# Optimization experiments

Measured on AMD Instinct MI355X. Metric: run time of the kernel, lower is better.

## Reference

```python
import jax, jax.numpy as jnp
import numpy as np

B, N, T, CIN, HID, EMB, K = 32, 256, 13, 2, 64, 10, 2


def setup_inputs() -> dict:
    key = jax.random.key(0)
    ks = jax.random.split(key, 24)
    r = lambda i, shape, s=1.0: jax.random.normal(ks[i], shape, jnp.float32) * s
    return {
        "times": jnp.arange(T, dtype=jnp.float32),
        # natural cubic spline coefficients: (B, N, T-1, CIN)
        "coeff_a": r(0, (B, N, T - 1, CIN)),
        "coeff_b": r(1, (B, N, T - 1, CIN), 0.1),
        "coeff_two_c": r(2, (B, N, T - 1, CIN), 0.1),
        "coeff_three_d": r(3, (B, N, T - 1, CIN), 0.1),
        # initial_h / initial_z linear layers (input -> hidden)
        "W_h": r(4, (CIN, HID), 0.5), "b_h": r(5, (HID,), 0.1),
        "W_z": r(6, (CIN, HID), 0.5), "b_z": r(7, (HID,), 0.1),
        # func_f (FinalTanh_f): linear_in, one hidden linear, linear_out -> hidden*input
        "Wf_in": r(8, (HID, HID), 0.1), "bf_in": r(9, (HID,), 0.05),
        "Wf_hid": r(10, (HID, HID), 0.1), "bf_hid": r(11, (HID,), 0.05),
        "Wf_out": r(12, (HID, HID * CIN), 0.1), "bf_out": r(13, (HID * CIN,), 0.05),
        # func_g (VectorField_g, g_type='agc')
        "Wg_in": r(14, (HID, HID), 0.1), "bg_in": r(15, (HID,), 0.05),
        "Eg": r(16, (N, EMB)),
        "W_pool": r(17, (EMB, K, HID, HID), 0.1),
        "b_pool": r(18, (EMB, HID), 0.1),
        "Wg_out": r(19, (HID, HID * CIN), 0.1), "bg_out": r(20, (HID * CIN,), 0.05),
    }


def reference(times, coeff_a, coeff_b, coeff_two_c, coeff_three_d,
              W_h, b_h, W_z, b_z,
              Wf_in, bf_in, Wf_hid, bf_hid, Wf_out, bf_out,
              Wg_in, bg_in, Eg, W_pool, b_pool, Wg_out, bg_out):
    maxidx = coeff_b.shape[-2] - 1

    def dX_dt(t):  # NaturalCubicSpline.derivative
        idx = jnp.clip(jnp.searchsorted(times, t, side='right') - 1, 0, maxidx)
        frac = t - times[idx]
        b = coeff_b[..., idx, :]
        c = coeff_two_c[..., idx, :]
        d = coeff_three_d[..., idx, :]
        return b + (c + d * frac) * frac  # (B, N, CIN)

    # adaptive graph conv (agc) static pieces, cheb_k = 2
    A = jax.nn.softmax(jax.nn.relu(Eg @ Eg.T), axis=1)          # (N, N)
    supports = jnp.stack([jnp.eye(N, dtype=A.dtype), A])        # (K, N, N)
    Wn = jnp.einsum('nd,dkio->nkio', Eg, W_pool)                # (N, K, HID, HID)
    bn = Eg @ b_pool                                            # (N, HID)

    def func_f(h):  # FinalTanh_f: MLP -> (B, N, HID, CIN) field
        x = jax.nn.relu(h @ Wf_in + bf_in)
        x = jax.nn.relu(x @ Wf_hid + bf_hid)
        x = (x @ Wf_out + bf_out).reshape(*x.shape[:-1], HID, CIN)
        return jnp.tanh(x)

    def func_g(z):  # VectorField_g with agc
        x = jax.nn.relu(z @ Wg_in + bg_in)                       # (B, N, HID)
        x_g = jnp.einsum('knm,bmc->bnkc', supports, x)           # (B, N, K, HID)
        x = jnp.einsum('bnki,nkio->bno', x_g, Wn) + bn           # (B, N, HID)
        x = (x @ Wg_out + bg_out).reshape(*x.shape[:-1], HID, CIN)
        return jnp.tanh(x)

    def vf(t, h, z):  # VectorField_g_dev of cdeint_gde_dev
        dX = dX_dt(t)                                            # (B, N, CIN)
        f = func_f(h)
        g = func_g(z)
        dh = jnp.einsum('bnhi,bni->bnh', f, dX)
        dz = jnp.einsum('bnhi,bni->bnh', g * f, dX)
        return dh, dz

    # spline.evaluate(times[0]) == coeff_a[..., 0, :] (frac = 0)
    x0 = coeff_a[..., 0, :]
    h0 = x0 @ W_h + b_h
    z0 = x0 @ W_z + b_z

    third = jnp.float32(1.0 / 3.0)

    def step(carry, ts):  # torchdiffeq 'rk4' (3/8 rule), one step per interval
        h, z = carry
        t0, t1 = ts
        dt = t1 - t0
        k1h, k1z = vf(t0, h, z)
        k2h, k2z = vf(t0 + dt * third, h + dt * third * k1h, z + dt * third * k1z)
        k3h, k3z = vf(t0 + dt * 2 * third, h + dt * (k2h - third * k1h), z + dt * (k2z - third * k1z))
        k4h, k4z = vf(t1, h + dt * (k1h - k2h + k3h), z + dt * (k1z - k2z + k3z))
        h = h + dt * 0.125 * (k1h + 3.0 * (k2h + k3h) + k4h)
        z = z + dt * 0.125 * (k1z + 3.0 * (k2z + k3z) + k4z)
        return (h, z), z

    ts = jnp.stack([times[:-1], times[1:]], axis=1)              # (T-1, 2)
    (_, _), z_seq = jax.lax.scan(step, (h0, z0), ts)
    z_t = jnp.concatenate([z0[None], z_seq], axis=0)             # (T, B, N, HID)
    return jnp.transpose(z_t, (1, 2, 0, 3))                      # (B, N, T, HID)
```

## Files before the change

### kernel.cpp

```cpp
#include <hip/hip_runtime.h>

typedef unsigned short ushort_t;
typedef unsigned int uint_t;

#define CW_OFF  0
#define A_OFF   524288
#define BN_OFF  786432
#define WN_OFF  851968
#define XB_OFF  5046272
#define H_OFF   7143424
#define Z_OFF   9240576
#define K1H_OFF 11337728
#define K1Z_OFF 13434880
#define K2H_OFF 15532032
#define K2Z_OFF 17629184
#define UH_OFF  19726336

#define F_X0     0
#define F_WH     16384
#define F_BH     16512
#define F_WZ     16576
#define F_BZ     16704
#define F_WFIN   16768
#define F_BFIN   20864
#define F_WFHID  20928
#define F_BFHID  25024
#define F_WFOUT  25088
#define F_BFOUT  33280
#define F_WGIN   33408
#define F_BGIN   37504
#define F_WGOUT  37568
#define F_BGOUT  45760
#define F_EG     45888
#define F_WPOOL  48448
#define F_BPOOL  130368

__device__ __forceinline__ float bfl(uint_t u){ union{uint_t i; float f;} c; c.i = u<<16; return c.f; }
__device__ __forceinline__ float bfh(uint_t u){ union{uint_t i; float f;} c; c.i = u & 0xffff0000u; return c.f; }
__device__ __forceinline__ float bf1(ushort_t u){ union{uint_t i; float f;} c; c.i = ((uint_t)u)<<16; return c.f; }
__device__ __forceinline__ uint_t f2bf(float x){
  uint_t u = __float_as_uint(x);
  uint_t r = u + 0x7fffu + ((u >> 16) & 1u);
  return r >> 16;
}
__device__ __forceinline__ float fast_tanh(float x){
  float e = __expf(2.0f*x);
  return 1.0f - 2.0f/(e+1.0f);
}
__device__ __forceinline__ bool inputs_are_f32(const void* times){
  return ((const uint_t*)times)[0] != 0x3F800000u;
}

__device__ __forceinline__ void dotf_4(const float* act, const float* W, int o0, float acc[4]) {
  const float4* a4 = (const float4*)act;
  #pragma unroll
  for (int i4 = 0; i4 < 16; ++i4) {
    float4 av4 = a4[i4];
    float av[4] = {av4.x, av4.y, av4.z, av4.w};
    #pragma unroll
    for (int ii = 0; ii < 4; ++ii) {
      float4 w = *(const float4*)(W + (i4*4+ii)*64 + o0);
      acc[0] += av[ii]*w.x; acc[1] += av[ii]*w.y;
      acc[2] += av[ii]*w.z; acc[3] += av[ii]*w.w;
    }
  }
}

__device__ __forceinline__ void dotf_8(const float* act, const float* W, int co0, float acc[8]) {
  const float4* a4 = (const float4*)act;
  #pragma unroll
  for (int i4 = 0; i4 < 16; ++i4) {
    float4 av4 = a4[i4];
    float av[4] = {av4.x, av4.y, av4.z, av4.w};
    #pragma unroll
    for (int ii = 0; ii < 4; ++ii) {
      const float* wp = W + (i4*4+ii)*128 + co0;
      float4 w0 = *(const float4*)(wp);
      float4 w1 = *(const float4*)(wp + 4);
      float a = av[ii];
      acc[0] += a*w0.x; acc[1] += a*w0.y; acc[2] += a*w0.z; acc[3] += a*w0.w;
      acc[4] += a*w1.x; acc[5] += a*w1.y; acc[6] += a*w1.z; acc[7] += a*w1.w;
    }
  }
}

__global__ __launch_bounds__(256) void k_conv(
    const void* times, const void* ca,
    const void* W_h, const void* b_h, const void* W_z, const void* b_z,
    const void* Wf_in, const void* bf_in, const void* Wf_hid, const void* bf_hid,
    const void* Wf_out, const void* bf_out, const void* Wg_in, const void* bg_in,
    const void* Wg_out, const void* bg_out, const void* Eg, const void* W_pool,
    const void* b_pool, char* __restrict__ wsb)
{
  const bool f32in = inputs_are_f32(times);
  float* F = (float*)(wsb + CW_OFF);
  if (blockIdx.x == 0) {
    for (int i = threadIdx.x; i < 16384; i += 256) {
      int si = (i >> 1)*24 + (i & 1);
      F[F_X0 + i] = f32in ? ((const float*)ca)[si] : bf1(((const ushort_t*)ca)[si]);
    }
    return;
  }
  const void* src = nullptr; int dst = 0, cnt = 0;
  switch (blockIdx.x) {
    case 1:  src = W_h;    dst = F_WH;    cnt = 128;   break;
    case 2:  src = b_h;    dst = F_BH;    cnt = 64;    break;
    case 3:  src = W_z;    dst = F_WZ;    cnt = 128;   break;
    case 4:  src = b_z;    dst = F_BZ;    cnt = 64;    break;
    case 5:  src = Wf_in;  dst = F_WFIN;  cnt = 4096;  break;
    case 6:  src = bf_in;  dst = F_BFIN;  cnt = 64;    break;
    case 7:  src = Wf_hid; dst = F_WFHID; cnt = 4096;  break;
    case 8:  src = bf_hid; dst = F_BFHID; cnt = 64;    break;
    case 9:  src = Wf_out; dst = F_WFOUT; cnt = 8192;  break;
    case 10: src = bf_out; dst = F_BFOUT; cnt = 128;   break;
    case 11: src = Wg_in;  dst = F_WGIN;  cnt = 4096;  break;
    case 12: src = bg_in;  dst = F_BGIN;  cnt = 64;    break;
    case 13: src = Wg_out; dst = F_WGOUT; cnt = 8192;  break;
    case 14: src = bg_out; dst = F_BGOUT; cnt = 128;   break;
    case 15: src = Eg;     dst = F_EG;    cnt = 2560;  break;
    case 16: src = W_pool; dst = F_WPOOL; cnt = 81920; break;
    default: src = b_pool; dst = F_BPOOL; cnt = 640;   break;
  }
  for (int i = threadIdx.x; i < cnt; i += 256)
    F[dst + i] = f32in ? ((const float*)src)[i] : bf1(((const ushort_t*)src)[i]);
}

__global__ __launch_bounds__(256) void k_A(char* __restrict__ wsb) {
  const float* F = (const float*)(wsb + CW_OFF);
  float* Aw = (float*)(wsb + A_OFF);
  float* bn = (float*)(wsb + BN_OFF);
  const int nrow = blockIdx.x;
  const int m = threadIdx.x;
  float eg_n[10];
  #pragma unroll
  for (int d = 0; d < 10; ++d) eg_n[d] = F[F_EG + nrow*10 + d];
  float dot = 0.f;
  #pragma unroll
  for (int d = 0; d < 10; ++d) dot += eg_n[d] * F[F_EG + m*10 + d];
  float v = fmaxf(dot, 0.f);
  __shared__ float red[256];
  red[m] = v; __syncthreads();
  for (int off = 128; off > 0; off >>= 1) {
    if (m < off) red[m] = fmaxf(red[m], red[m+off]);
    __syncthreads();
  }
  float vmax = red[0]; __syncthreads();
  float e = __expf(v - vmax);
  red[m] = e; __syncthreads();
  for (int off = 128; off > 0; off >>= 1) {
    if (m < off) red[m] += red[m+off];
    __syncthreads();
  }
  float ssum = red[0];
  Aw[nrow*256 + m] = e / ssum;
  if (m < 64) {
    float acc = 0.f;
    #pragma unroll
    for (int d = 0; d < 10; ++d) acc += eg_n[d] * F[F_BPOOL + d*64 + m];
    bn[nrow*64 + m] = acc;
  }
}

__global__ __launch_bounds__(256) void k_Wn(char* __restrict__ wsb) {
  const float* F = (const float*)(wsb + CW_OFF);
  ushort_t* Wn = (ushort_t*)(wsb + WN_OFF);
  int idx = blockIdx.x*256 + threadIdx.x;
  int o = idx & 63;
  int i = (idx >> 6) & 63;
  int k = (idx >> 12) & 1;
  int n = idx >> 13;
  float acc = 0.f;
  #pragma unroll
  for (int d = 0; d < 10; ++d)
    acc += F[F_EG + n*10 + d] * F[F_WPOOL + ((d*2 + k)*64 + i)*64 + o];
  Wn[idx] = (ushort_t)f2bf(acc);
}

__global__ __launch_bounds__(512) void k_init2(char* __restrict__ wsb, float* __restrict__ out) {
  const float* F = (const float*)(wsb + CW_OFF);
  float* H = (float*)(wsb + H_OFF);
  float* Z = (float*)(wsb + Z_OFF);
  ushort_t* X0 = (ushort_t*)(wsb + XB_OFF);

  const int tid = threadIdx.x;
  const int lr  = tid >> 4;
  const int o0  = (tid & 15) * 4;
  const int row = blockIdx.x * 32 + lr;

  __shared__ __align__(16) float sIn[32][68];

  float a0 = F[F_X0 + row*2 + 0];
  float a1 = F[F_X0 + row*2 + 1];
  float h[4], z[4];
  #pragma unroll
  for (int j = 0; j < 4; ++j) {
    h[j] = a0*F[F_WH + o0+j] + a1*F[F_WH + 64+o0+j] + F[F_BH + o0+j];
    z[j] = a0*F[F_WZ + o0+j] + a1*F[F_WZ + 64+o0+j] + F[F_BZ + o0+j];
  }
  *(float4*)(H + row*64 + o0) = make_float4(h[0],h[1],h[2],h[3]);
  *(float4*)(Z + row*64 + o0) = make_float4(z[0],z[1],z[2],z[3]);
  *(float4*)(out + (row*13)*64 + o0) = make_float4(z[0],z[1],z[2],z[3]);

  *(float4*)&sIn[lr][o0] = make_float4(z[0],z[1],z[2],z[3]);
  __syncthreads();
  float xr[4];
  { float4 bv = *(const float4*)(F + F_BGIN + o0);
    xr[0]=bv.x; xr[1]=bv.y; xr[2]=bv.z; xr[3]=bv.w; }
  dotf_4(&sIn[lr][0], F + F_WGIN, o0, xr);
  #pragma unroll
  for (int j=0;j<4;++j) xr[j] = fmaxf(xr[j], 0.f);
  { uint2 pk;
    pk.x = f2bf(xr[0]) | (f2bf(xr[1]) << 16);
    pk.y = f2bf(xr[2]) | (f2bf(xr[3]) << 16);
    *(uint2*)(X0 + row*64 + o0) = pk; }
}

__global__ __launch_bounds__(512) void k_stage(
    const void* __restrict__ times,
    const void* __restrict__ cbv, const void* __restrict__ ccv, const void* __restrict__ cdv,
    char* __restrict__ wsb, float* __restrict__ out, int vfc)
{
  const float* F  = (const float*)(wsb + CW_OFF);
  const float* Aw = (const float*)(wsb + A_OFF);
  const float* bn = (const float*)(wsb + BN_OFF);
  const ushort_t* Wn = (const ushort_t*)(wsb + WN_OFF);
  ushort_t* XB = (ushort_t*)(wsb + XB_OFF);
  float* H   = (float*)(wsb + H_OFF);
  float* Z   = (float*)(wsb + Z_OFF);
  float* K1h = (float*)(wsb + K1H_OFF);
  float* K1z = (float*)(wsb + K1Z_OFF);
  float* K2h = (float*)(wsb + K2H_OFF);
  float* K2z = (float*)(wsb + K2Z_OFF);
  float* UH  = (float*)(wsb + UH_OFF);
  const bool f32in = inputs_are_f32(times);

  const int s  = vfc >> 2;
  const int st = vfc & 3;
  const ushort_t* Xc = XB + (vfc & 1) * 524288;
  ushort_t*       Xn = XB + ((vfc + 1) & 1) * 524288;

  const int tid = threadIdx.x;
  const int lr  = tid >> 4;
  const int t16 = tid & 15;
  const int o0  = t16 * 4;
  const int co0 = o0 * 2;
  const int bb  = blockIdx.x >> 3;
  const int nr  = blockIdx.x & 7;
  const int n   = nr * 32 + lr;
  const int row = bb * 256 + n;

  __shared__ __align__(16) float sIn[32][68];
  __shared__ __align__(16) float sT [32][68];
  __shared__ __align__(16) float sX [32][68];
  __shared__ __align__(16) float xs [128][68];

  { uint2 w = *(const uint2*)(Xc + row*64 + o0);
    *(float4*)&sX[lr][o0] = make_float4(bfl(w.x), bfh(w.x), bfl(w.y), bfh(w.y)); }

  float y[4] = {0.f,0.f,0.f,0.f};
  const float* Arow = Aw + n*256;
  #pragma unroll 1
  for (int half = 0; half < 2; ++half) {
    __syncthreads();
    #pragma unroll
    for (int q = tid; q < 2048; q += 512) {
      int r = q >> 4, c4 = q & 15;
      uint2 w = *(const uint2*)(Xc + (bb*256 + half*128 + r)*64 + c4*4);
      *(float4*)&xs[r][c4*4] = make_float4(bfl(w.x), bfh(w.x), bfl(w.y), bfh(w.y));
    }
    __syncthreads();
    #pragma unroll 4
    for (int m4 = 0; m4 < 32; ++m4) {
      float4 av = *(const float4*)(Arow + half*128 + m4*4);
      float am[4] = {av.x, av.y, av.z, av.w};
      #pragma unroll
      for (int mm = 0; mm < 4; ++mm) {
        float4 xv = *(const float4*)&xs[m4*4+mm][o0];
        y[0] += am[mm]*xv.x; y[1] += am[mm]*xv.y;
        y[2] += am[mm]*xv.z; y[3] += am[mm]*xv.w;
      }
    }
  }

  __syncthreads();
  *(float4*)&sT[lr][o0] = make_float4(y[0],y[1],y[2],y[3]);
  __syncthreads();
  float og[4];
  { float4 bv = *(const float4*)(bn + n*64 + o0); og[0]=bv.x; og[1]=bv.y; og[2]=bv.z; og[3]=bv.w; }
  const ushort_t* W0 = Wn + n*8192;
  #pragma unroll
  for (int i4 = 0; i4 < 16; ++i4) {
    float4 xa = *(const float4*)&sX[lr][i4*4];
    float4 ya = *(const float4*)&sT[lr][i4*4];
    float xav[4]={xa.x,xa.y,xa.z,xa.w};
    float yav[4]={ya.x,ya.y,ya.z,ya.w};
    #pragma unroll
    for (int ii = 0; ii < 4; ++ii) {
      int i = i4*4 + ii;
      uint2 w0 = *(const uint2*)(W0 + i*64 + o0);
      uint2 w1 = *(const uint2*)(W0 + 4096 + i*64 + o0);
      og[0] += xav[ii]*bfl(w0.x) + yav[ii]*bfl(w1.x);
      og[1] += xav[ii]*bfh(w0.x) + yav[ii]*bfh(w1.x);
      og[2] += xav[ii]*bfl(w0.y) + yav[ii]*bfl(w1.y);
      og[3] += xav[ii]*bfh(w0.y) + yav[ii]*bfh(w1.y);
    }
  }
  *(float4*)&sIn[lr][o0] = make_float4(og[0],og[1],og[2],og[3]);
  __syncthreads();
  float go[8];
  { float4 b0 = *(const float4*)(F + F_BGOUT + co0);
    float4 b1 = *(const float4*)(F + F_BGOUT + co0 + 4);
    go[0]=b0.x; go[1]=b0.y; go[2]=b0.z; go[3]=b0.w;
    go[4]=b1.x; go[5]=b1.y; go[6]=b1.z; go[7]=b1.w; }
  dotf_8(&sIn[lr][0], F + F_WGOUT, co0, go);
  float g0[4], g1[4];
  #pragma unroll
  for (int j=0;j<4;++j){ g0[j]=fast_tanh(go[2*j]); g1[j]=fast_tanh(go[2*j+1]); }

  __syncthreads();
  { const float* UHsrc = (st == 0) ? H : UH;
    float4 uv = *(const float4*)(UHsrc + row*64 + o0);
    *(float4*)&sIn[lr][o0] = uv; }
  __syncthreads();
  float a1v[4];
  { float4 bv = *(const float4*)(F + F_BFIN + o0);
    a1v[0]=bv.x; a1v[1]=bv.y; a1v[2]=bv.z; a1v[3]=bv.w; }
  dotf_4(&sIn[lr][0], F + F_WFIN, o0, a1v);
  #pragma unroll
  for (int j=0;j<4;++j) a1v[j] = fmaxf(a1v[j], 0.f);
  *(float4*)&sT[lr][o0] = make_float4(a1v[0],a1v[1],a1v[2],a1v[3]);
  __syncthreads();
  float a2v[4];
  { float4 bv = *(const float4*)(F + F_BFHID + o0);
    a2v[0]=bv.x; a2v[1]=bv.y; a2v[2]=bv.z; a2v[3]=bv.w; }
  dotf_4(&sT[lr][0], F + F_WFHID, o0, a2v);
  #pragma unroll
  for (int j=0;j<4;++j) a2v[j] = fmaxf(a2v[j], 0.f);
  *(float4*)&sIn[lr][o0] = make_float4(a2v[0],a2v[1],a2v[2],a2v[3]);
  __syncthreads();
  float fo[8];
  { float4 b0 = *(const float4*)(F + F_BFOUT + co0);
    float4 b1 = *(const float4*)(F + F_BFOUT + co0 + 4);
    fo[0]=b0.x; fo[1]=b0.y; fo[2]=b0.z; fo[3]=b0.w;
    fo[4]=b1.x; fo[5]=b1.y; fo[6]=b1.z; fo[7]=b1.w; }
  dotf_8(&sIn[lr][0], F + F_WFOUT, co0, fo);
  float f0[4], f1[4];
  #pragma unroll
  for (int j=0;j<4;++j){ f0[j]=fast_tanh(fo[2*j]); f1[j]=fast_tanh(fo[2*j+1]); }

  int sidx; float frac;
  if (st == 0)      { sidx = s; frac = 0.f; }
  else if (st == 1) { sidx = s; frac = 0.33333334f; }
  else if (st == 2) { sidx = s; frac = 0.66666669f; }
  else              { sidx = (s < 11) ? s+1 : 11; frac = (s < 11) ? 0.f : 1.f; }
  float dX0, dX1;
  if (f32in) {
    float2 vb = *(const float2*)((const float*)cbv + (row*12 + sidx)*2);
    float2 vc = *(const float2*)((const float*)ccv + (row*12 + sidx)*2);
    float2 vd = *(const float2*)((const float*)cdv + (row*12 + sidx)*2);
    dX0 = vb.x + (vc.x + vd.x*frac)*frac;
    dX1 = vb.y + (vc.y + vd.y*frac)*frac;
  } else {
    uint_t vb = *(const uint_t*)((const ushort_t*)cbv + (row*12 + sidx)*2);
    uint_t vc = *(const uint_t*)((const ushort_t*)ccv + (row*12 + sidx)*2);
    uint_t vd = *(const uint_t*)((const ushort_t*)cdv + (row*12 + sidx)*2);
    dX0 = bfl(vb) + (bfl(vc) + bfl(vd)*frac)*frac;
    dX1 = bfh(vb) + (bfh(vc) + bfh(vd)*frac)*frac;
  }

  float dh[4], dz[4];
  #pragma unroll
  for (int j=0;j<4;++j){
    dh[j] = f0[j]*dX0 + f1[j]*dX1;
    dz[j] = g0[j]*f0[j]*dX0 + g1[j]*f1[j]*dX1;
  }

  float uh_n[4], uz_n[4];
  float4 hv = *(const float4*)(H + row*64 + o0);
  float4 zv = *(const float4*)(Z + row*64 + o0);
  float h[4] = {hv.x,hv.y,hv.z,hv.w};
  float z[4] = {zv.x,zv.y,zv.z,zv.w};

  if (st == 0) {
    *(float4*)(K1h + row*64 + o0) = make_float4(dh[0],dh[1],dh[2],dh[3]);
    *(float4*)(K1z + row*64 + o0) = make_float4(dz[0],dz[1],dz[2],dz[3]);
    #pragma unroll
    for (int j=0;j<4;++j){ uh_n[j]=h[j]+dh[j]*(1.f/3.f); uz_n[j]=z[j]+dz[j]*(1.f/3.f); }
  } else if (st == 1) {
    float4 k1hv = *(const float4*)(K1h + row*64 + o0);
    float4 k1zv = *(const float4*)(K1z + row*64 + o0);
    float k1hl[4]={k1hv.x,k1hv.y,k1hv.z,k1hv.w};
    float k1zl[4]={k1zv.x,k1zv.y,k1zv.z,k1zv.w};
    float Qh[4],Qz[4],Ph[4],Pz[4];
    #pragma unroll
    for (int j=0;j<4;++j){
      Qh[j]=k1hl[j]+3.f*dh[j]; Qz[j]=k1zl[j]+3.f*dz[j];
      Ph[j]=k1hl[j]-dh[j];     Pz[j]=k1zl[j]-dz[j];
      uh_n[j]=h[j]+dh[j]-k1hl[j]*(1.f/3.f);
      uz_n[j]=z[j]+dz[j]-k1zl[j]*(1.f/3.f);
    }
    *(float4*)(K1h + row*64 + o0) = make_float4(Qh[0],Qh[1],Qh[2],Qh[3]);
    *(float4*)(K1z + row*64 + o0) = make_float4(Qz[0],Qz[1],Qz[2],Qz[3]);
    *(float4*)(K2h + row*64 + o0) = make_float4(Ph[0],Ph[1],Ph[2],Ph[3]);
    *(float4*)(K2z + row*64 + o0) = make_float4(Pz[0],Pz[1],Pz[2],Pz[3]);
  } else if (st == 2) {
    float4 Qhv = *(const float4*)(K1h + row*64 + o0);
    float4 Qzv = *(const float4*)(K1z + row*64 + o0);
    float4 Phv = *(const float4*)(K2h + row*64 + o0);
    float4 Pzv = *(const float4*)(K2z + row*64 + o0);
    float Qh[4]={Qhv.x,Qhv.y,Qhv.z,Qhv.w}, Qz[4]={Qzv.x,Qzv.y,Qzv.z,Qzv.w};
    float Ph[4]={Phv.x,Phv.y,Phv.z,Phv.w}, Pz[4]={Pzv.x,Pzv.y,Pzv.z,Pzv.w};
    float Ah[4],Az[4];
    #pragma unroll
    for (int j=0;j<4;++j){
      Ah[j]=Qh[j]+3.f*dh[j]; Az[j]=Qz[j]+3.f*dz[j];
      uh_n[j]=h[j]+Ph[j]+dh[j];
      uz_n[j]=z[j]+Pz[j]+dz[j];
    }
    *(float4*)(K1h + row*64 + o0) = make_float4(Ah[0],Ah[1],Ah[2],Ah[3]);
    *(float4*)(K1z + row*64 + o0) = make_float4(Az[0],Az[1],Az[2],Az[3]);
  } else {
    float4 Ahv = *(const float4*)(K1h + row*64 + o0);
    float4 Azv = *(const float4*)(K1z + row*64 + o0);
    #pragma unroll
    for (int j=0;j<4;++j){
      float hn = h[j] + 0.125f*(((const float*)&Ahv)[j] + dh[j]);
      float zn = z[j] + 0.125f*(((const float*)&Azv)[j] + dz[j]);
      uh_n[j]=hn; uz_n[j]=zn;
    }
    *(float4*)(H + row*64 + o0) = make_float4(uh_n[0],uh_n[1],uh_n[2],uh_n[3]);
    *(float4*)(Z + row*64 + o0) = make_float4(uz_n[0],uz_n[1],uz_n[2],uz_n[3]);
    *(float4*)(out + (row*13 + s + 1)*64 + o0) = make_float4(uz_n[0],uz_n[1],uz_n[2],uz_n[3]);
  }

  if (vfc < 47) {
    *(float4*)(UH + row*64 + o0) = make_float4(uh_n[0],uh_n[1],uh_n[2],uh_n[3]);
    __syncthreads();
    *(float4*)&sIn[lr][o0] = make_float4(uz_n[0],uz_n[1],uz_n[2],uz_n[3]);
    __syncthreads();
    float xr[4];
    { float4 bv = *(const float4*)(F + F_BGIN + o0);
      xr[0]=bv.x; xr[1]=bv.y; xr[2]=bv.z; xr[3]=bv.w; }
    dotf_4(&sIn[lr][0], F + F_WGIN, o0, xr);
    #pragma unroll
    for (int j=0;j<4;++j) xr[j] = fmaxf(xr[j], 0.f);
    uint2 pk;
    pk.x = f2bf(xr[0]) | (f2bf(xr[1]) << 16);
    pk.y = f2bf(xr[2]) | (f2bf(xr[3]) << 16);
    *(uint2*)(Xn + row*64 + o0) = pk;
  }
}

extern "C" void kernel_launch(void* const* d_in, const int* in_sizes, int n_in,
                              void* d_out, int out_size, void* d_ws, size_t ws_size,
                              hipStream_t stream) {
  const void* times   = d_in[0];
  const void* coeff_a = d_in[1];
  const void* coeff_b = d_in[2];
  const void* coeff_c = d_in[3];
  const void* coeff_d = d_in[4];
  const void* W_h    = d_in[5];
  const void* b_h    = d_in[6];
  const void* W_z    = d_in[7];
  const void* b_z    = d_in[8];
  const void* Wf_in  = d_in[9];
  const void* bf_in  = d_in[10];
  const void* Wf_hid = d_in[11];
  const void* bf_hid = d_in[12];
  const void* Wf_out = d_in[13];
  const void* bf_out = d_in[14];
  const void* Wg_in  = d_in[15];
  const void* bg_in  = d_in[16];
  const void* Eg     = d_in[17];
  const void* W_pool = d_in[18];
  const void* b_pool = d_in[19];
  const void* Wg_out = d_in[20];
  const void* bg_out = d_in[21];

  char* wsb = (char*)d_ws;
  float* out = (float*)d_out;

  hipLaunchKernelGGL(k_conv, dim3(18), dim3(256), 0, stream,
                     times, coeff_a, W_h, b_h, W_z, b_z,
                     Wf_in, bf_in, Wf_hid, bf_hid, Wf_out, bf_out,
                     Wg_in, bg_in, Wg_out, bg_out, Eg, W_pool, b_pool, wsb);
  hipLaunchKernelGGL(k_A,  dim3(256),  dim3(256), 0, stream, wsb);
  hipLaunchKernelGGL(k_Wn, dim3(8192), dim3(256), 0, stream, wsb);
  hipLaunchKernelGGL(k_init2, dim3(256), dim3(512), 0, stream, wsb, out);
  for (int vfc = 0; vfc < 48; ++vfc) {
    hipLaunchKernelGGL(k_stage, dim3(256), dim3(512), 0, stream,
                       times, coeff_b, coeff_c, coeff_d, wsb, out, vfc);
  }
}
```

Before: 5.216 ms.

## Claim stage tiles per XCD via atomic flags and use nontemporal stores

Each k_stage block reads its hardware XCD id and claims a (batch, node-range) tile with atomicCAS on a per-tile flag array. This keeps a given tile on the same XCD across the 48 stage launches so its L2-resident state (H, Z, K buffers) is reused. It also switches write-once or read-once buffers (out, K2h/K2z) to nontemporal loads and stores to reduce cache pollution. The cost is a serialized atomic claim at the start of every block, plus a dependence on the workspace being large enough and on the flag counters staying in step with vfc.

```diff
diff --git a/kernel.cpp b/kernel.cpp
--- a/kernel.cpp
+++ b/kernel.cpp
@@ -2,6 +2,7 @@
 
 typedef unsigned short ushort_t;
 typedef unsigned int uint_t;
+typedef float f4v __attribute__((ext_vector_type(4)));
 
 #define CW_OFF  0
 #define A_OFF   524288
@@ -15,6 +16,8 @@
 #define K2H_OFF 15532032
 #define K2Z_OFF 17629184
 #define UH_OFF  19726336
+#define FLAGS_OFF 21823488
+#define WS_NEED   21824512
 
 #define F_X0     0
 #define F_WH     16384
@@ -51,6 +54,12 @@
   return ((const uint_t*)times)[0] != 0x3F800000u;
 }
 
+__device__ __forceinline__ f4v ntld4(const float* p){ return __builtin_nontemporal_load((const f4v*)p); }
+__device__ __forceinline__ void ntst4(float* p, float a, float b, float c, float d){
+  f4v v; v[0]=a; v[1]=b; v[2]=c; v[3]=d;
+  __builtin_nontemporal_store(v, (f4v*)p);
+}
+
 __device__ __forceinline__ void dotf_4(const float* act, const float* W, int o0, float acc[4]) {
   const float4* a4 = (const float4*)act;
   #pragma unroll
@@ -90,11 +99,15 @@
     const void* Wf_in, const void* bf_in, const void* Wf_hid, const void* bf_hid,
     const void* Wf_out, const void* bf_out, const void* Wg_in, const void* bg_in,
     const void* Wg_out, const void* bg_out, const void* Eg, const void* W_pool,
-    const void* b_pool, char* __restrict__ wsb)
+    const void* b_pool, char* __restrict__ wsb, int claim_en)
 {
   const bool f32in = inputs_are_f32(times);
   float* F = (float*)(wsb + CW_OFF);
   if (blockIdx.x == 0) {
+    if (claim_en) {
+      int* flags = (int*)(wsb + FLAGS_OFF);
+      for (int i = threadIdx.x; i < 256; i += 256) flags[i] = 0;
+    }
     for (int i = threadIdx.x; i < 16384; i += 256) {
       int si = (i >> 1)*24 + (i & 1);
       F[F_X0 + i] = f32in ? ((const float*)ca)[si] : bf1(((const ushort_t*)ca)[si]);
@@ -199,7 +212,7 @@
   }
   *(float4*)(H + row*64 + o0) = make_float4(h[0],h[1],h[2],h[3]);
   *(float4*)(Z + row*64 + o0) = make_float4(z[0],z[1],z[2],z[3]);
-  *(float4*)(out + (row*13)*64 + o0) = make_float4(z[0],z[1],z[2],z[3]);
+  ntst4(out + (row*13)*64 + o0, z[0],z[1],z[2],z[3]);
 
   *(float4*)&sIn[lr][o0] = make_float4(z[0],z[1],z[2],z[3]);
   __syncthreads();
@@ -218,7 +231,7 @@
 __global__ __launch_bounds__(512) void k_stage(
     const void* __restrict__ times,
     const void* __restrict__ cbv, const void* __restrict__ ccv, const void* __restrict__ cdv,
-    char* __restrict__ wsb, float* __restrict__ out, int vfc)
+    char* __restrict__ wsb, float* __restrict__ out, int vfc, int claim_en)
 {
   const float* F  = (const float*)(wsb + CW_OFF);
   const float* Aw = (const float*)(wsb + A_OFF);
@@ -244,8 +257,38 @@
   const int t16 = tid & 15;
   const int o0  = t16 * 4;
   const int co0 = o0 * 2;
-  const int bb  = blockIdx.x >> 3;
-  const int nr  = blockIdx.x & 7;
+
+  int bb, nr;
+  __shared__ int s_slot;
+  if (claim_en) {
+    if (tid == 0) {
+      int* flags = (int*)(wsb + FLAGS_OFF);
+      uint_t x = __builtin_amdgcn_s_getreg((3 << 11) | 20) & 7u;
+      int slot = -1;
+      int start = (int)(blockIdx.x >> 3) & 31;
+      #pragma unroll 1
+      for (int t = 0; t < 32; ++t) {
+        int s2 = (((start + t) & 31) << 3) | (int)x;
+        if (atomicCAS(&flags[s2], vfc, vfc + 1) == vfc) { slot = s2; break; }
+      }
+      #pragma unroll 1
+      while (slot < 0) {
+        #pragma unroll 1
+        for (int t = 0; t < 256; ++t) {
+          int s2 = ((int)blockIdx.x + t) & 255;
+          if (atomicCAS(&flags[s2], vfc, vfc + 1) == vfc) { slot = s2; break; }
+        }
+      }
+      s_slot = slot;
+    }
+    __syncthreads();
+    bb = s_slot >> 3;
+    nr = s_slot & 7;
+  } else {
+    bb = blockIdx.x >> 3;
+    nr = blockIdx.x & 7;
+  }
+
   const int n   = nr * 32 + lr;
   const int row = bb * 256 + n;
 
@@ -401,15 +444,15 @@
     }
     *(float4*)(K1h + row*64 + o0) = make_float4(Qh[0],Qh[1],Qh[2],Qh[3]);
     *(float4*)(K1z + row*64 + o0) = make_float4(Qz[0],Qz[1],Qz[2],Qz[3]);
-    *(float4*)(K2h + row*64 + o0) = make_float4(Ph[0],Ph[1],Ph[2],Ph[3]);
-    *(float4*)(K2z + row*64 + o0) = make_float4(Pz[0],Pz[1],Pz[2],Pz[3]);
+    ntst4(K2h + row*64 + o0, Ph[0],Ph[1],Ph[2],Ph[3]);
+    ntst4(K2z + row*64 + o0, Pz[0],Pz[1],Pz[2],Pz[3]);
   } else if (st == 2) {
     float4 Qhv = *(const float4*)(K1h + row*64 + o0);
     float4 Qzv = *(const float4*)(K1z + row*64 + o0);
-    float4 Phv = *(const float4*)(K2h + row*64 + o0);
-    float4 Pzv = *(const float4*)(K2z + row*64 + o0);
+    f4v Phv = ntld4(K2h + row*64 + o0);
+    f4v Pzv = ntld4(K2z + row*64 + o0);
     float Qh[4]={Qhv.x,Qhv.y,Qhv.z,Qhv.w}, Qz[4]={Qzv.x,Qzv.y,Qzv.z,Qzv.w};
-    float Ph[4]={Phv.x,Phv.y,Phv.z,Phv.w}, Pz[4]={Pzv.x,Pzv.y,Pzv.z,Pzv.w};
+    float Ph[4]={Phv[0],Phv[1],Phv[2],Phv[3]}, Pz[4]={Pzv[0],Pzv[1],Pzv[2],Pzv[3]};
     float Ah[4],Az[4];
     #pragma unroll
     for (int j=0;j<4;++j){
@@ -430,7 +473,7 @@
     }
     *(float4*)(H + row*64 + o0) = make_float4(uh_n[0],uh_n[1],uh_n[2],uh_n[3]);
     *(float4*)(Z + row*64 + o0) = make_float4(uz_n[0],uz_n[1],uz_n[2],uz_n[3]);
-    *(float4*)(out + (row*13 + s + 1)*64 + o0) = make_float4(uz_n[0],uz_n[1],uz_n[2],uz_n[3]);
+    ntst4(out + (row*13 + s + 1)*64 + o0, uz_n[0],uz_n[1],uz_n[2],uz_n[3]);
   }
 
   if (vfc < 47) {
@@ -479,16 +522,17 @@
 
   char* wsb = (char*)d_ws;
   float* out = (float*)d_out;
+  const int claim_en = (ws_size >= (size_t)WS_NEED) ? 1 : 0;
 
   hipLaunchKernelGGL(k_conv, dim3(18), dim3(256), 0, stream,
                      times, coeff_a, W_h, b_h, W_z, b_z,
                      Wf_in, bf_in, Wf_hid, bf_hid, Wf_out, bf_out,
-                     Wg_in, bg_in, Wg_out, bg_out, Eg, W_pool, b_pool, wsb);
+                     Wg_in, bg_in, Wg_out, bg_out, Eg, W_pool, b_pool, wsb, claim_en);
   hipLaunchKernelGGL(k_A,  dim3(256),  dim3(256), 0, stream, wsb);
   hipLaunchKernelGGL(k_Wn, dim3(8192), dim3(256), 0, stream, wsb);
   hipLaunchKernelGGL(k_init2, dim3(256), dim3(512), 0, stream, wsb, out);
   for (int vfc = 0; vfc < 48; ++vfc) {
     hipLaunchKernelGGL(k_stage, dim3(256), dim3(512), 0, stream,
-                       times, coeff_b, coeff_c, coeff_d, wsb, out, vfc);
-  }
-}
+                       times, coeff_b, coeff_c, coeff_d, wsb, out, vfc, claim_en);
+  }
+}
```

After: 5.146 ms. No clear change (-1.3%).

## Remap stage blocks to XCC-local work slots via atomic claims; use nontemporal output stores

Applied to the files above, without the earlier changes.

Each k_stage block reads its XCC id from a hardware register and atomically claims a (batch, node-range) slot whose low bits match that XCC. This keeps each slot on the same XCC across the 48 stage launches so its working set stays in that XCC's L2. Output stores become nontemporal so the write-once output does not evict reused data. The cost is an atomic claim loop at block start, plus a fallback scan when no matching slot is free.

```diff
diff --git a/kernel.cpp b/kernel.cpp
--- a/kernel.cpp
+++ b/kernel.cpp
@@ -2,6 +2,7 @@
 
 typedef unsigned short ushort_t;
 typedef unsigned int uint_t;
+typedef float f4v __attribute__((ext_vector_type(4)));
 
 #define CW_OFF  0
 #define A_OFF   524288
@@ -35,6 +36,8 @@
 #define F_WPOOL  48448
 #define F_BPOOL  130368
 
+__device__ int g_claim[256];
+
 __device__ __forceinline__ float bfl(uint_t u){ union{uint_t i; float f;} c; c.i = u<<16; return c.f; }
 __device__ __forceinline__ float bfh(uint_t u){ union{uint_t i; float f;} c; c.i = u & 0xffff0000u; return c.f; }
 __device__ __forceinline__ float bf1(ushort_t u){ union{uint_t i; float f;} c; c.i = ((uint_t)u)<<16; return c.f; }
@@ -49,6 +52,11 @@
 }
 __device__ __forceinline__ bool inputs_are_f32(const void* times){
   return ((const uint_t*)times)[0] != 0x3F800000u;
+}
+
+__device__ __forceinline__ void ntst4(float* p, float a, float b, float c, float d){
+  f4v v; v[0]=a; v[1]=b; v[2]=c; v[3]=d;
+  __builtin_nontemporal_store(v, (f4v*)p);
 }
 
 __device__ __forceinline__ void dotf_4(const float* act, const float* W, int o0, float acc[4]) {
@@ -95,6 +103,7 @@
   const bool f32in = inputs_are_f32(times);
   float* F = (float*)(wsb + CW_OFF);
   if (blockIdx.x == 0) {
+    if (threadIdx.x < 256) g_claim[threadIdx.x] = 0;
     for (int i = threadIdx.x; i < 16384; i += 256) {
       int si = (i >> 1)*24 + (i & 1);
       F[F_X0 + i] = f32in ? ((const float*)ca)[si] : bf1(((const ushort_t*)ca)[si]);
@@ -199,7 +208,7 @@
   }
   *(float4*)(H + row*64 + o0) = make_float4(h[0],h[1],h[2],h[3]);
   *(float4*)(Z + row*64 + o0) = make_float4(z[0],z[1],z[2],z[3]);
-  *(float4*)(out + (row*13)*64 + o0) = make_float4(z[0],z[1],z[2],z[3]);
+  ntst4(out + (row*13)*64 + o0, z[0],z[1],z[2],z[3]);
 
   *(float4*)&sIn[lr][o0] = make_float4(z[0],z[1],z[2],z[3]);
   __syncthreads();
@@ -244,8 +253,32 @@
   const int t16 = tid & 15;
   const int o0  = t16 * 4;
   const int co0 = o0 * 2;
-  const int bb  = blockIdx.x >> 3;
-  const int nr  = blockIdx.x & 7;
+
+  int bb, nr;
+  __shared__ int s_slot;
+  if (tid == 0) {
+    uint_t x = __builtin_amdgcn_s_getreg((3 << 11) | 20) & 7u;
+    int slot = -1;
+    int start = (int)(blockIdx.x >> 3) & 31;
+    #pragma unroll 1
+    for (int t = 0; t < 32; ++t) {
+      int s2 = (((start + t) & 31) << 3) | (int)x;
+      if (atomicCAS(&g_claim[s2], vfc, vfc + 1) == vfc) { slot = s2; break; }
+    }
+    #pragma unroll 1
+    while (slot < 0) {
+      #pragma unroll 1
+      for (int t = 0; t < 256; ++t) {
+        int s2 = ((int)blockIdx.x + t) & 255;
+        if (atomicCAS(&g_claim[s2], vfc, vfc + 1) == vfc) { slot = s2; break; }
+      }
+    }
+    s_slot = slot;
+  }
+  __syncthreads();
+  bb = s_slot >> 3;
+  nr = s_slot & 7;
+
   const int n   = nr * 32 + lr;
   const int row = bb * 256 + n;
 
@@ -430,7 +463,7 @@
     }
     *(float4*)(H + row*64 + o0) = make_float4(uh_n[0],uh_n[1],uh_n[2],uh_n[3]);
     *(float4*)(Z + row*64 + o0) = make_float4(uz_n[0],uz_n[1],uz_n[2],uz_n[3]);
-    *(float4*)(out + (row*13 + s + 1)*64 + o0) = make_float4(uz_n[0],uz_n[1],uz_n[2],uz_n[3]);
+    ntst4(out + (row*13 + s + 1)*64 + o0, uz_n[0],uz_n[1],uz_n[2],uz_n[3]);
   }
 
   if (vfc < 47) {
```

Result: faster. 5.086 ms (-2.5%).

## Factor per-node weight pool through embedding instead of materializing Wn

Applied to the files above, without the earlier changes.

Replaces the precomputed per-node bf16 weight tensor Wn (N*K*64*64) with on-the-fly contraction against the shared W_pool (EMB*K*64*64), which is packed as bf16 pairs. Each stage accumulates 10 partial sums, one per embedding dimension, using bf16 dot2 instructions, then combines them with the node's embedding. This removes per-node weight streaming from memory, which was about 4MB per stage, in exchange for roughly 5x more ALU work and more registers. It also parallelizes the conversion kernel across more blocks and uses nontemporal stores for the output.

```diff
diff --git a/kernel.cpp b/kernel.cpp
--- a/kernel.cpp
+++ b/kernel.cpp
@@ -2,6 +2,17 @@
 
 typedef unsigned short ushort_t;
 typedef unsigned int uint_t;
+typedef float f4v __attribute__((ext_vector_type(4)));
+typedef short bf16x2 __attribute__((ext_vector_type(2)));
+
+#if defined(__has_builtin)
+#if __has_builtin(__builtin_amdgcn_fdot2_f32_bf16)
+#define HAVE_DOT2 1
+#endif
+#endif
+#ifndef HAVE_DOT2
+#define HAVE_DOT2 0
+#endif
 
 #define CW_OFF  0
 #define A_OFF   524288
@@ -43,12 +54,18 @@
   uint_t r = u + 0x7fffu + ((u >> 16) & 1u);
   return r >> 16;
 }
+__device__ __forceinline__ bf16x2 u2bf(uint_t u){ union{uint_t i; bf16x2 v;} c; c.i = u; return c.v; }
 __device__ __forceinline__ float fast_tanh(float x){
   float e = __expf(2.0f*x);
   return 1.0f - 2.0f/(e+1.0f);
 }
 __device__ __forceinline__ bool inputs_are_f32(const void* times){
   return ((const uint_t*)times)[0] != 0x3F800000u;
+}
+
+__device__ __forceinline__ void ntst4(float* p, float a, float b, float c, float d){
+  f4v v; v[0]=a; v[1]=b; v[2]=c; v[3]=d;
+  __builtin_nontemporal_store(v, (f4v*)p);
 }
 
 __device__ __forceinline__ void dotf_4(const float* act, const float* W, int o0, float acc[4]) {
@@ -81,6 +98,16 @@
       acc[0] += a*w0.x; acc[1] += a*w0.y; acc[2] += a*w0.z; acc[3] += a*w0.w;
       acc[4] += a*w1.x; acc[5] += a*w1.y; acc[6] += a*w1.z; acc[7] += a*w1.w;
     }
+  }
+}
+
+__device__ __forceinline__ void cvt_copy(float* dst, const void* src, int cnt, bool f32in){
+  if (f32in) {
+    const float* s = (const float*)src;
+    for (int i = threadIdx.x; i < cnt; i += 256) dst[i] = s[i];
+  } else {
+    const ushort_t* s = (const ushort_t*)src;
+    for (int i = threadIdx.x; i < cnt; i += 256) dst[i] = bf1(s[i]);
   }
 }
 
@@ -94,35 +121,51 @@
 {
   const bool f32in = inputs_are_f32(times);
   float* F = (float*)(wsb + CW_OFF);
-  if (blockIdx.x == 0) {
-    for (int i = threadIdx.x; i < 16384; i += 256) {
-      int si = (i >> 1)*24 + (i & 1);
-      F[F_X0 + i] = f32in ? ((const float*)ca)[si] : bf1(((const ushort_t*)ca)[si]);
+  const int bid = blockIdx.x;
+  if (bid < 4) {
+    const int base = bid * 4096;
+    if (f32in) {
+      const float* s = (const float*)ca;
+      for (int i = threadIdx.x; i < 4096; i += 256) {
+        int g = base + i;
+        F[F_X0 + g] = s[(g >> 1)*24 + (g & 1)];
+      }
+    } else {
+      const ushort_t* s = (const ushort_t*)ca;
+      for (int i = threadIdx.x; i < 4096; i += 256) {
+        int g = base + i;
+        F[F_X0 + g] = bf1(s[(g >> 1)*24 + (g & 1)]);
+      }
     }
     return;
   }
+  if (bid < 20) {
+    const int off = (bid - 4) * 5120;
+    const void* srcp = f32in ? (const void*)((const float*)W_pool + off)
+                             : (const void*)((const ushort_t*)W_pool + off);
+    cvt_copy(F + F_WPOOL + off, srcp, 5120, f32in);
+    return;
+  }
   const void* src = nullptr; int dst = 0, cnt = 0;
-  switch (blockIdx.x) {
-    case 1:  src = W_h;    dst = F_WH;    cnt = 128;   break;
-    case 2:  src = b_h;    dst = F_BH;    cnt = 64;    break;
-    case 3:  src = W_z;    dst = F_WZ;    cnt = 128;   break;
-    case 4:  src = b_z;    dst = F_BZ;    cnt = 64;    break;
-    case 5:  src = Wf_in;  dst = F_WFIN;  cnt = 4096;  break;
-    case 6:  src = bf_in;  dst = F_BFIN;  cnt = 64;    break;
-    case 7:  src = Wf_hid; dst = F_WFHID; cnt = 4096;  break;
-    case 8:  src = bf_hid; dst = F_BFHID; cnt = 64;    break;
-    case 9:  src = Wf_out; dst = F_WFOUT; cnt = 8192;  break;
-    case 10: src = bf_out; dst = F_BFOUT; cnt = 128;   break;
-    case 11: src = Wg_in;  dst = F_WGIN;  cnt = 4096;  break;
-    case 12: src = bg_in;  dst = F_BGIN;  cnt = 64;    break;
-    case 13: src = Wg_out; dst = F_WGOUT; cnt = 8192;  break;
-    case 14: src = bg_out; dst = F_BGOUT; cnt = 128;   break;
-    case 15: src = Eg;     dst = F_EG;    cnt = 2560;  break;
-    case 16: src = W_pool; dst = F_WPOOL; cnt = 81920; break;
-    default: src = b_pool; dst = F_BPOOL; cnt = 640;   break;
-  }
-  for (int i = threadIdx.x; i < cnt; i += 256)
-    F[dst + i] = f32in ? ((const float*)src)[i] : bf1(((const ushort_t*)src)[i]);
+  switch (bid) {
+    case 20: src = W_h;    dst = F_WH;    cnt = 128;  break;
+    case 21: src = b_h;    dst = F_BH;    cnt = 64;   break;
+    case 22: src = W_z;    dst = F_WZ;    cnt = 128;  break;
+    case 23: src = b_z;    dst = F_BZ;    cnt = 64;   break;
+    case 24: src = Wf_in;  dst = F_WFIN;  cnt = 4096; break;
+    case 25: src = bf_in;  dst = F_BFIN;  cnt = 64;   break;
+    case 26: src = Wf_hid; dst = F_WFHID; cnt = 4096; break;
+    case 27: src = bf_hid; dst = F_BFHID; cnt = 64;   break;
+    case 28: src = Wf_out; dst = F_WFOUT; cnt = 8192; break;
+    case 29: src = bf_out; dst = F_BFOUT; cnt = 128;  break;
+    case 30: src = Wg_in;  dst = F_WGIN;  cnt = 4096; break;
+    case 31: src = bg_in;  dst = F_BGIN;  cnt = 64;   break;
+    case 32: src = Wg_out; dst = F_WGOUT; cnt = 8192; break;
+    case 33: src = bg_out; dst = F_BGOUT; cnt = 128;  break;
+    case 34: src = Eg;     dst = F_EG;    cnt = 2560; break;
+    default: src = b_pool; dst = F_BPOOL; cnt = 640;  break;
+  }
+  cvt_copy(F + dst, src, cnt, f32in);
 }
 
 __global__ __launch_bounds__(256) void k_A(char* __restrict__ wsb) {
@@ -161,19 +204,18 @@
   }
 }
 
-__global__ __launch_bounds__(256) void k_Wn(char* __restrict__ wsb) {
+__global__ __launch_bounds__(256) void k_pack(char* __restrict__ wsb) {
   const float* F = (const float*)(wsb + CW_OFF);
-  ushort_t* Wn = (ushort_t*)(wsb + WN_OFF);
-  int idx = blockIdx.x*256 + threadIdx.x;
-  int o = idx & 63;
-  int i = (idx >> 6) & 63;
-  int k = (idx >> 12) & 1;
-  int n = idx >> 13;
-  float acc = 0.f;
-  #pragma unroll
-  for (int d = 0; d < 10; ++d)
-    acc += F[F_EG + n*10 + d] * F[F_WPOOL + ((d*2 + k)*64 + i)*64 + o];
-  Wn[idx] = (ushort_t)f2bf(acc);
+  uint_t* WPK = (uint_t*)(wsb + WN_OFF);
+  int u0 = blockIdx.x * 1024 + threadIdx.x;
+  #pragma unroll
+  for (int t = 0; t < 4; ++t) {
+    int u = u0 + t*256;
+    int d = u >> 12, rem = u & 4095;
+    float w0 = F[F_WPOOL + d*8192 + rem];
+    float w1 = F[F_WPOOL + d*8192 + 4096 + rem];
+    WPK[u] = f2bf(w0) | (f2bf(w1) << 16);
+  }
 }
 
 __global__ __launch_bounds__(512) void k_init2(char* __restrict__ wsb, float* __restrict__ out) {
@@ -199,7 +241,7 @@
   }
   *(float4*)(H + row*64 + o0) = make_float4(h[0],h[1],h[2],h[3]);
   *(float4*)(Z + row*64 + o0) = make_float4(z[0],z[1],z[2],z[3]);
-  *(float4*)(out + (row*13)*64 + o0) = make_float4(z[0],z[1],z[2],z[3]);
+  ntst4(out + (row*13)*64 + o0, z[0],z[1],z[2],z[3]);
 
   *(float4*)&sIn[lr][o0] = make_float4(z[0],z[1],z[2],z[3]);
   __syncthreads();
@@ -223,7 +265,7 @@
   const float* F  = (const float*)(wsb + CW_OFF);
   const float* Aw = (const float*)(wsb + A_OFF);
   const float* bn = (const float*)(wsb + BN_OFF);
-  const ushort_t* Wn = (const ushort_t*)(wsb + WN_OFF);
+  const uint_t* WPK = (const uint_t*)(wsb + WN_OFF);
   ushort_t* XB = (ushort_t*)(wsb + XB_OFF);
   float* H   = (float*)(wsb + H_OFF);
   float* Z   = (float*)(wsb + Z_OFF);
@@ -285,10 +327,13 @@
   __syncthreads();
   *(float4*)&sT[lr][o0] = make_float4(y[0],y[1],y[2],y[3]);
   __syncthreads();
-  float og[4];
-  { float4 bv = *(const float4*)(bn + n*64 + o0); og[0]=bv.x; og[1]=bv.y; og[2]=bv.z; og[3]=bv.w; }
-  const ushort_t* W0 = Wn + n*8192;
-  #pragma unroll
+  float eg_n[10];
+  #pragma unroll
+  for (int d = 0; d < 10; ++d) eg_n[d] = F[F_EG + n*10 + d];
+  float tacc[10][4];
+  #pragma unroll
+  for (int d = 0; d < 10; ++d) { tacc[d][0]=0.f; tacc[d][1]=0.f; tacc[d][2]=0.f; tacc[d][3]=0.f; }
+  #pragma unroll 2
   for (int i4 = 0; i4 < 16; ++i4) {
     float4 xa = *(const float4*)&sX[lr][i4*4];
     float4 ya = *(const float4*)&sT[lr][i4*4];
@@ -296,14 +341,36 @@
     float yav[4]={ya.x,ya.y,ya.z,ya.w};
     #pragma unroll
     for (int ii = 0; ii < 4; ++ii) {
-      int i = i4*4 + ii;
-      uint2 w0 = *(const uint2*)(W0 + i*64 + o0);
-      uint2 w1 = *(const uint2*)(W0 + 4096 + i*64 + o0);
-      og[0] += xav[ii]*bfl(w0.x) + yav[ii]*bfl(w1.x);
-      og[1] += xav[ii]*bfh(w0.x) + yav[ii]*bfh(w1.x);
-      og[2] += xav[ii]*bfl(w0.y) + yav[ii]*bfl(w1.y);
-      og[3] += xav[ii]*bfh(w0.y) + yav[ii]*bfh(w1.y);
-    }
+      const int i = i4*4 + ii;
+#if HAVE_DOT2
+      bf16x2 xyv = u2bf(f2bf(xav[ii]) | (f2bf(yav[ii]) << 16));
+      #pragma unroll
+      for (int d = 0; d < 10; ++d) {
+        uint4 w = *(const uint4*)(WPK + ((d*64 + i) << 6) + o0);
+        tacc[d][0] = __builtin_amdgcn_fdot2_f32_bf16(xyv, u2bf(w.x), tacc[d][0], false);
+        tacc[d][1] = __builtin_amdgcn_fdot2_f32_bf16(xyv, u2bf(w.y), tacc[d][1], false);
+        tacc[d][2] = __builtin_amdgcn_fdot2_f32_bf16(xyv, u2bf(w.z), tacc[d][2], false);
+        tacc[d][3] = __builtin_amdgcn_fdot2_f32_bf16(xyv, u2bf(w.w), tacc[d][3], false);
+      }
+#else
+      float xs_ = xav[ii], ys_ = yav[ii];
+      #pragma unroll
+      for (int d = 0; d < 10; ++d) {
+        uint4 w = *(const uint4*)(WPK + ((d*64 + i) << 6) + o0);
+        tacc[d][0] += xs_*bfl(w.x) + ys_*bfh(w.x);
+        tacc[d][1] += xs_*bfl(w.y) + ys_*bfh(w.y);
+        tacc[d][2] += xs_*bfl(w.z) + ys_*bfh(w.z);
+        tacc[d][3] += xs_*bfl(w.w) + ys_*bfh(w.w);
+      }
+#endif
+    }
+  }
+  float og[4];
+  { float4 bv = *(const float4*)(bn + n*64 + o0); og[0]=bv.x; og[1]=bv.y; og[2]=bv.z; og[3]=bv.w; }
+  #pragma unroll
+  for (int d = 0; d < 10; ++d) {
+    og[0] += eg_n[d]*tacc[d][0]; og[1] += eg_n[d]*tacc[d][1];
+    og[2] += eg_n[d]*tacc[d][2]; og[3] += eg_n[d]*tacc[d][3];
   }
   *(float4*)&sIn[lr][o0] = make_float4(og[0],og[1],og[2],og[3]);
   __syncthreads();
@@ -430,7 +497,7 @@
     }
     *(float4*)(H + row*64 + o0) = make_float4(uh_n[0],uh_n[1],uh_n[2],uh_n[3]);
     *(float4*)(Z + row*64 + o0) = make_float4(uz_n[0],uz_n[1],uz_n[2],uz_n[3]);
-    *(float4*)(out + (row*13 + s + 1)*64 + o0) = make_float4(uz_n[0],uz_n[1],uz_n[2],uz_n[3]);
+    ntst4(out + (row*13 + s + 1)*64 + o0, uz_n[0],uz_n[1],uz_n[2],uz_n[3]);
   }
 
   if (vfc < 47) {
@@ -480,12 +547,12 @@
   char* wsb = (char*)d_ws;
   float* out = (float*)d_out;
 
-  hipLaunchKernelGGL(k_conv, dim3(18), dim3(256), 0, stream,
+  hipLaunchKernelGGL(k_conv, dim3(36), dim3(256), 0, stream,
                      times, coeff_a, W_h, b_h, W_z, b_z,
                      Wf_in, bf_in, Wf_hid, bf_hid, Wf_out, bf_out,
                      Wg_in, bg_in, Wg_out, bg_out, Eg, W_pool, b_pool, wsb);
-  hipLaunchKernelGGL(k_A,  dim3(256),  dim3(256), 0, stream, wsb);
-  hipLaunchKernelGGL(k_Wn, dim3(8192), dim3(256), 0, stream, wsb);
+  hipLaunchKernelGGL(k_A,    dim3(256), dim3(256), 0, stream, wsb);
+  hipLaunchKernelGGL(k_pack, dim3(40),  dim3(256), 0, stream, wsb);
   hipLaunchKernelGGL(k_init2, dim3(256), dim3(512), 0, stream, wsb, out);
   for (int vfc = 0; vfc < 48; ++vfc) {
     hipLaunchKernelGGL(k_stage, dim3(256), dim3(512), 0, stream,
```

After: 13.39 ms. +156.6%, slower.
